# Kernel optimization log

Measured on AMD Instinct MI355X. Metric: run time of the kernel, lower is better.

## Reference

```python
import jax, jax.numpy as jnp
import numpy as np

L = 5          # num_layer
D = 300        # emb_dim
N = 100000     # nodes
E = 250000     # edges
G = 4000       # graphs
EPS = 1e-5


def setup_inputs() -> dict:
    key = jax.random.key(0)
    ks = jax.random.split(key, 32)
    f = lambda k, shape, s=0.02: (jax.random.normal(k, shape, dtype=jnp.float32) * s)
    inp = {
        "x_atom": jax.random.randint(ks[0], (N,), 0, 120),
        "x_chir": jax.random.randint(ks[1], (N,), 0, 3),
        "src": jax.random.randint(ks[2], (E,), 0, N),
        "dst": jax.random.randint(ks[3], (E,), 0, N),
        "edge_type": jax.random.randint(ks[4], (E,), 0, 6),
        "edge_dir": jax.random.randint(ks[5], (E,), 0, 3),
        "batch": jnp.sort(jax.random.randint(ks[6], (N,), 0, G)),
        # node feature embeddings
        "x_emb1": f(ks[7], (120, D), 0.1),
        "x_emb2": f(ks[8], (3, D), 0.1),
        # per-layer GIN params (stacked over L)
        "edge_e1": f(ks[9], (L, 6, D), 0.1),
        "edge_e2": f(ks[10], (L, 3, D), 0.1),
        "mlp_w1": f(ks[11], (L, D, 2 * D)),
        "mlp_b1": jnp.zeros((L, 2 * D), jnp.float32),
        "mlp_w2": f(ks[12], (L, 2 * D, D)),
        "mlp_b2": jnp.zeros((L, D), jnp.float32),
        # BatchNorm (inference mode: running stats)
        "bn_gamma": jnp.ones((L, D), jnp.float32),
        "bn_beta": jnp.zeros((L, D), jnp.float32),
        "bn_mean": f(ks[13], (L, D), 0.1),
        "bn_var": jax.random.uniform(ks[14], (L, D), jnp.float32, 0.5, 1.5),
        # virtual node (embedding initialized to zero in the original)
        "vn_emb": jnp.zeros((D,), jnp.float32),
        # vn MLPs: Linear -> LayerNorm -> ReLU -> Linear, L-1 of them
        "vn_w1": f(ks[15], (L - 1, D, D)),
        "vn_b1": jnp.zeros((L - 1, D), jnp.float32),
        "vn_ln_g": jnp.ones((L - 1, D), jnp.float32),
        "vn_ln_b": jnp.zeros((L - 1, D), jnp.float32),
        "vn_w2": f(ks[16], (L - 1, D, D)),
        "vn_b2": jnp.zeros((L - 1, D), jnp.float32),
    }
    return inp


def _forward(x_atom, x_chir, src, dst, edge_type, edge_dir, batch,
             x_emb1, x_emb2, edge_e1, edge_e2, mlp_w1, mlp_b1, mlp_w2, mlp_b2,
             bn_gamma, bn_beta, bn_mean, bn_var,
             vn_emb, vn_w1, vn_b1, vn_ln_g, vn_ln_b, vn_w2, vn_b2):
    n = x_atom.shape[0]
    # node counts per graph for mean pooling (guard empty graphs)
    counts = jnp.maximum(
        jax.ops.segment_sum(jnp.ones((n, 1), jnp.float32), batch, num_segments=G), 1.0)

    h = x_emb1[x_atom] + x_emb2[x_chir]                      # [N, D]
    vn_h = jnp.broadcast_to(vn_emb, (G, D))                  # [G, D]
    h = h + vn_h[batch]

    for l in range(L):
        # --- GIN conv: message = h[src] + edge_emb, scatter-add to dst ---
        edge_emb = edge_e1[l][edge_type] + edge_e2[l][edge_dir]   # [E, D]
        msg = h[src] + edge_emb
        aggr = jax.ops.segment_sum(msg, dst, num_segments=n)      # [N, D]
        # self loops: x_j = h[i], self-loop attr = (type 4, dir 0)
        aggr = aggr + h + (edge_e1[l][4] + edge_e2[l][0])
        # MLP: Linear(D,2D) -> ReLU -> Linear(2D,D)
        z = jax.nn.relu(aggr @ mlp_w1[l] + mlp_b1[l]) @ mlp_w2[l] + mlp_b2[l]
        # BatchNorm1d (eval): running stats
        z = (z - bn_mean[l]) * (bn_gamma[l] * jax.lax.rsqrt(bn_var[l] + EPS)) + bn_beta[l]
        if l < L - 1:
            z = jax.nn.relu(z)  # (dropout is identity at inference)
            # --- virtual node update ---
            pooled = jax.ops.segment_sum(z, batch, num_segments=G) / counts
            vn_new = pooled + vn_h                                # [G, D]
            t = vn_new @ vn_w1[l] + vn_b1[l]
            mu = jnp.mean(t, axis=-1, keepdims=True)
            var = jnp.var(t, axis=-1, keepdims=True)
            t = (t - mu) * jax.lax.rsqrt(var + EPS) * vn_ln_g[l] + vn_ln_b[l]
            vn_h = jax.nn.relu(t) @ vn_w2[l] + vn_b2[l]
            z = z + vn_h[batch]
        h = z
    return h


def reference(x_atom, x_chir, src, dst, edge_type, edge_dir, batch,
              x_emb1, x_emb2, edge_e1, edge_e2, mlp_w1, mlp_b1, mlp_w2, mlp_b2,
              bn_gamma, bn_beta, bn_mean, bn_var,
              vn_emb, vn_w1, vn_b1, vn_ln_g, vn_ln_b, vn_w2, vn_b2):
    return _forward(x_atom, x_chir, src, dst, edge_type, edge_dir, batch,
                    x_emb1, x_emb2, edge_e1, edge_e2, mlp_w1, mlp_b1, mlp_w2, mlp_b2,
                    bn_gamma, bn_beta, bn_mean, bn_var,
                    vn_emb, vn_w1, vn_b1, vn_ln_g, vn_ln_b, vn_w2, vn_b2)
```

## Files before the change

kernel.cpp:

```cpp
#include <hip/hip_runtime.h>

#define DD   300
#define DD2  600
#define GG   4000
#define GPAD 4096
#define LL   5
#define BN_EPS 1e-5f

typedef float f32x4  __attribute__((ext_vector_type(4)));
typedef short bf16x8 __attribute__((ext_vector_type(8)));

__device__ __forceinline__ unsigned short f2bf(float f) {
    unsigned int x = __float_as_uint(f);
    unsigned int r = (x + 0x7FFFu + ((x >> 16) & 1u)) >> 16;
    return (unsigned short)r;
}

__global__ __launch_bounds__(256) void k_hist(const int* __restrict__ idx, int* __restrict__ cnt, int n) {
    int i = blockIdx.x * 256 + threadIdx.x;
    if (i < n) atomicAdd(&cnt[idx[i]], 1);
}

__global__ __launch_bounds__(256) void k_scan1(const int* __restrict__ in, int* __restrict__ bsum, int n) {
    int t = threadIdx.x;
    int i = blockIdx.x * 256 + t;
    int v = (i < n) ? in[i] : 0;
    for (int off = 32; off >= 1; off >>= 1) v += __shfl_down(v, off, 64);
    __shared__ int s[4];
    if ((t & 63) == 0) s[t >> 6] = v;
    __syncthreads();
    if (t == 0) bsum[blockIdx.x] = s[0] + s[1] + s[2] + s[3];
}
__global__ __launch_bounds__(1024) void k_scan2(int* __restrict__ bsum, int nb) {
    __shared__ int s[1024];
    int t = threadIdx.x;
    int v = (t < nb) ? bsum[t] : 0;
    s[t] = v;
    __syncthreads();
    for (int off = 1; off < 1024; off <<= 1) {
        int u = (t >= off) ? s[t - off] : 0;
        __syncthreads();
        s[t] += u;
        __syncthreads();
    }
    if (t < nb) bsum[t] = s[t] - v;
}
__global__ __launch_bounds__(256) void k_scan3(const int* __restrict__ in, const int* __restrict__ boff,
                                               int* __restrict__ out, int n, int total) {
    __shared__ int s[256];
    int t = threadIdx.x;
    int i = blockIdx.x * 256 + t;
    int v = (i < n) ? in[i] : 0;
    s[t] = v;
    __syncthreads();
    for (int off = 1; off < 256; off <<= 1) {
        int u = (t >= off) ? s[t - off] : 0;
        __syncthreads();
        s[t] += u;
        __syncthreads();
    }
    if (i < n) out[i] = boff[blockIdx.x] + s[t] - v;
    if (i == 0) out[n] = total;
}

__global__ __launch_bounds__(256) void k_place(const int* __restrict__ src, const int* __restrict__ dst,
                                               const int* __restrict__ ety, const int* __restrict__ edir,
                                               const int* __restrict__ rowptr, int* __restrict__ cursor,
                                               int* __restrict__ einfo, int E) {
    int e = blockIdx.x * 256 + threadIdx.x;
    if (e >= E) return;
    int d = dst[e];
    int pos = rowptr[d] + atomicAdd(&cursor[d], 1);
    einfo[pos] = src[e] | ((ety[e] * 3 + edir[e]) << 20);
}

__global__ __launch_bounds__(256) void k_comb(const float* __restrict__ e1, const float* __restrict__ e2,
                                              float* __restrict__ comb) {
    int c = blockIdx.x, l = blockIdx.y;
    const float* r1 = e1 + ((size_t)l * 6 + (c / 3)) * DD;
    const float* r2 = e2 + ((size_t)l * 3 + (c % 3)) * DD;
    float* out = comb + ((size_t)l * 18 + c) * DD;
    for (int d = threadIdx.x; d < DD; d += 256) out[d] = r1[d] + r2[d];
}

__global__ __launch_bounds__(256) void k_init_h(const int* __restrict__ xa, const int* __restrict__ xc,
                                                const float* __restrict__ emb1, const float* __restrict__ emb2,
                                                const float* __restrict__ vne,
                                                float* __restrict__ h, int N) {
    int n = blockIdx.x;
    if (n >= N) return;
    int a = xa[n], c = xc[n];
    for (int d = threadIdx.x; d < DD; d += 256)
        h[(size_t)n * DD + d] = emb1[(size_t)a * DD + d] + emb2[(size_t)c * DD + d] + vne[d];
}

__global__ __launch_bounds__(256) void k_init_vn(const float* __restrict__ vne, float* __restrict__ vnh) {
    int g = blockIdx.x;
    for (int d = threadIdx.x; d < DD; d += 256) vnh[(size_t)g * DD + d] = vne[d];
}

__global__ __launch_bounds__(256) void k_aggr(const float* __restrict__ h,
                                              const int* __restrict__ rowptr, const int* __restrict__ einfo,
                                              const float* __restrict__ comb,
                                              const int* __restrict__ batch, const float* __restrict__ vnh,
                                              int use_vn,
                                              unsigned short* __restrict__ aggrb, int N, int Npad) {
    const int node = blockIdx.x * 4 + (threadIdx.x >> 6);
    const int lane = threadIdx.x & 63;
    if (node >= Npad) return;
    unsigned short* out = aggrb + (size_t)node * 320;
    if (node >= N) {
#pragma unroll
        for (int j = 0; j < 5; j++) out[lane + 64 * j] = 0;
        return;
    }
    float acc[5];
    const float* sc = comb + 12 * DD;
    const int p0 = rowptr[node], p1 = rowptr[node + 1];
    if (use_vn) {
        {
            const float* hs = h + (size_t)node * DD;
            const float* vs = vnh + (size_t)batch[node] * DD;
#pragma unroll
            for (int j = 0; j < 5; j++) {
                int d = lane + 64 * j;
                acc[j] = (d < DD) ? hs[d] + sc[d] + vs[d] : 0.f;
            }
        }
        for (int p = p0; p < p1; p++) {
            int info = einfo[p];
            int s = info & 0xFFFFF;
            const float* hr = h + (size_t)s * DD;
            const float* cr = comb + (size_t)(info >> 20) * DD;
            const float* vr = vnh + (size_t)batch[s] * DD;
#pragma unroll
            for (int j = 0; j < 5; j++) {
                int d = lane + 64 * j;
                if (d < DD) acc[j] += hr[d] + cr[d] + vr[d];
            }
        }
    } else {
        {
            const float* hs = h + (size_t)node * DD;
#pragma unroll
            for (int j = 0; j < 5; j++) {
                int d = lane + 64 * j;
                acc[j] = (d < DD) ? hs[d] + sc[d] : 0.f;
            }
        }
        for (int p = p0; p < p1; p++) {
            int info = einfo[p];
            const float* hr = h + (size_t)(info & 0xFFFFF) * DD;
            const float* cr = comb + (size_t)(info >> 20) * DD;
#pragma unroll
            for (int j = 0; j < 5; j++) {
                int d = lane + 64 * j;
                if (d < DD) acc[j] += hr[d] + cr[d];
            }
        }
    }
#pragma unroll
    for (int j = 0; j < 5; j++) {
        int d = lane + 64 * j;
        out[d] = (d < DD) ? f2bf(acc[j]) : (unsigned short)0;
    }
}

__global__ __launch_bounds__(256) void k_convw(const float* __restrict__ w, short* __restrict__ wt,
                                               int K, int Nn, int KP, int NP) {
    int n = blockIdx.x;
    int l = blockIdx.y;
    const float* wl = w + (size_t)l * K * Nn;
    short* wtl = wt + (size_t)l * NP * KP;
    for (int k = threadIdx.x; k < KP; k += 256) {
        float v = (k < K && n < Nn) ? wl[(size_t)k * Nn + n] : 0.f;
        wtl[(size_t)n * KP + k] = (short)f2bf(v);
    }
}

__global__ __launch_bounds__(256) void k_padb(const float* __restrict__ b, float* __restrict__ bp) {
    int l = blockIdx.y;
    int n = blockIdx.x * 256 + threadIdx.x;
    if (n < 640) bp[(size_t)l * 640 + n] = (n < DD2) ? b[(size_t)l * DD2 + n] : 0.f;
}


#define LD3(PTR, STRIDE, ROWBASE, KOFF)                                                                     \
    do {                                                                                                    \
        v0 = *(const float4*)((PTR) + (size_t)((ROWBASE) + (t >> 2)) * (STRIDE) + (KOFF) + (t & 3) * 8);    \
        v1 = *(const float4*)((PTR) + (size_t)((ROWBASE) + (t >> 2) + 64) * (STRIDE) + (KOFF) + (t & 3) * 8); \
        if (t < 128)                                                                                        \
            v2 = *(const float4*)((PTR) + (size_t)((ROWBASE) + (t >> 2) + 128) * (STRIDE) + (KOFF) + (t & 3) * 8); \
    } while (0)

#define ST3(BUF)                                                    \
    do {                                                            \
        *(float4*)&sB[BUF][t >> 2][(t & 3) * 8] = v0;               \
        *(float4*)&sB[BUF][(t >> 2) + 64][(t & 3) * 8] = v1;        \
        if (t < 128) *(float4*)&sB[BUF][(t >> 2) + 128][(t & 3) * 8] = v2; \
    } while (0)

__global__ __launch_bounds__(256, 2) void k_mlp(const unsigned short* __restrict__ aggrb,
                                                const short* __restrict__ w1t,
                                                const float* __restrict__ b1p,
                                                const short* __restrict__ w2t,
                                                const float* __restrict__ b2,
                                                const float* __restrict__ bng, const float* __restrict__ bnb,
                                                const float* __restrict__ bnm, const float* __restrict__ bnv,
                                                float* __restrict__ h, int N, int relu_out) {
    __shared__ short sH[64][168];
    __shared__ short sB[2][160][40];

    const int t    = threadIdx.x;
    const int m0   = blockIdx.x * 64;
    const int lane = t & 63;
    const int w    = t >> 6;
    const int col  = lane & 15;
    const int kq   = lane >> 4;
    const int kb   = kq << 3;
    const int mrow = (w << 4) + col;

    bf16x8 areg[10];
    {
        const unsigned short* ap = aggrb + (size_t)(m0 + mrow) * 320 + kb;
#pragma unroll
        for (int ks = 0; ks < 10; ks++)
            areg[ks] = *(const bf16x8*)(ap + ks * 32);
        float4 v0, v1, v2;
        LD3(w1t, 320, 0, 0);
        ST3(0);
    }
    __syncthreads();

    f32x4 zacc[20];
#pragma unroll
    for (int j = 0; j < 20; j++) zacc[j] = (f32x4){0.f, 0.f, 0.f, 0.f};

    for (int ch = 0; ch < 4; ch++) {
        f32x4 hacc[10];
#pragma unroll
        for (int j = 0; j < 10; j++) hacc[j] = (f32x4){0.f, 0.f, 0.f, 0.f};

#pragma unroll
        for (int ks = 0; ks < 10; ks++) {
            float4 v0, v1, v2;
            if (ks < 9) LD3(w1t, 320, ch * 160, (ks + 1) * 32);
            else        LD3(w2t, 640, 0, ch * 160);
#pragma unroll
            for (int nt = 0; nt < 10; nt++) {
                bf16x8 b = *(const bf16x8*)&sB[ks & 1][(nt << 4) + col][kb];
                hacc[nt] = __builtin_amdgcn_mfma_f32_16x16x32_bf16(areg[ks], b, hacc[nt], 0, 0, 0);
            }
            ST3((ks & 1) ^ 1);
            if (ks == 9) {
#pragma unroll
                for (int nt = 0; nt < 10; nt++) {
                    float bias = b1p[ch * 160 + (nt << 4) + col];
#pragma unroll
                    for (int r = 0; r < 4; r++)
                        sH[(w << 4) + (kq << 2) + r][(nt << 4) + col] =
                            (short)f2bf(fmaxf(hacc[nt][r] + bias, 0.f));
                }
            }
            __syncthreads();
        }

#pragma unroll
        for (int s = 0; s < 10; s++) {
            const int ks2 = s >> 1, half = s & 1;
            float4 v0, v1, v2;
            bool stage = true;
            if (s < 9)       LD3(w2t, 640, ((s + 1) & 1) * 160, ch * 160 + ((s + 1) >> 1) * 32);
            else if (ch < 3) LD3(w1t, 320, (ch + 1) * 160, 0);
            else stage = false;
            bf16x8 a = *(const bf16x8*)&sH[mrow][ks2 * 32 + kb];
#pragma unroll
            for (int jt = 0; jt < 10; jt++) {
                bf16x8 b = *(const bf16x8*)&sB[s & 1][(jt << 4) + col][kb];
                zacc[half * 10 + jt] = __builtin_amdgcn_mfma_f32_16x16x32_bf16(a, b, zacc[half * 10 + jt], 0, 0, 0);
            }
            if (stage) ST3((s & 1) ^ 1);
            __syncthreads();
        }
    }

#pragma unroll
    for (int j = 0; j < 20; j++) {
        int n = (j << 4) + col;
        if (n < DD) {
            float bz = b2[n];
            float sc = bng[n] * rsqrtf(bnv[n] + BN_EPS);
            float mB = bnm[n], bB = bnb[n];
            int mbase = m0 + (w << 4) + (kq << 2);
#pragma unroll
            for (int r = 0; r < 4; r++) {
                int m = mbase + r;
                if (m < N) {
                    float z = (zacc[j][r] + bz - mB) * sc + bB;
                    if (relu_out) z = fmaxf(z, 0.f);
                    h[(size_t)m * DD + n] = z;
                }
            }
        }
    }
}

__global__ __launch_bounds__(256) void k_pool2(const float* __restrict__ h, const int* __restrict__ gptr,
                                               const float* __restrict__ vnh,
                                               unsigned short* __restrict__ vnin) {
    int g = blockIdx.x, t = threadIdx.x;
    const int gs = gptr[g], ge = gptr[g + 1];
    const float inv = 1.0f / fmaxf((float)(ge - gs), 1.0f);
    const int j0 = t, j1 = t + 256;
    const bool g1 = (j1 < DD);
    float a0 = 0.f, a1 = 0.f;
    for (int n = gs; n < ge; n++) {
        a0 += h[(size_t)n * DD + j0];
        if (g1) a1 += h[(size_t)n * DD + j1];
    }
    vnin[(size_t)g * 320 + j0] = f2bf(a0 * inv + vnh[(size_t)g * DD + j0]);
    if (j1 < 320)
        vnin[(size_t)g * 320 + j1] = g1 ? f2bf(a1 * inv + vnh[(size_t)g * DD + j1]) : (unsigned short)0;
}

__global__ __launch_bounds__(256) void k_vng(const unsigned short* __restrict__ A,
                                             const short* __restrict__ Wt,
                                             const float* __restrict__ bias,
                                             float* __restrict__ outf,
                                             int M) {
    __shared__ short sA[2][64][40];
    __shared__ short sB[2][160][40];
    const int t  = threadIdx.x;
    const int m0 = blockIdx.x * 64;
    const int n0 = blockIdx.y * 160;
    const int ar = t >> 2, aq = (t & 3) << 3;

    {
        *(float4*)&sA[0][ar][aq] = *(const float4*)(A + (size_t)(m0 + ar) * 320 + aq);
#pragma unroll
        for (int i = 0; i < 3; i++) {
            int c = t + (i << 8);
            if (c < 640) {
                int br = c >> 2, bq = (c & 3) << 3;
                *(float4*)&sB[0][br][bq] = *(const float4*)(Wt + (size_t)(n0 + br) * 320 + bq);
            }
        }
    }
    __syncthreads();

    const int lane = t & 63;
    const int w    = t >> 6;
    const int mrow = (w << 4) + (lane & 15);
    const int kb   = (lane >> 4) << 3;
    const int col  = lane & 15;
    const int rq   = (lane >> 4) << 2;

    f32x4 acc[10];
#pragma unroll
    for (int nt = 0; nt < 10; nt++) acc[nt] = (f32x4){0.f, 0.f, 0.f, 0.f};

    for (int ks = 0; ks < 10; ks++) {
        const int nb = ks & 1;
        const bool have = (ks + 1) < 10;
        float4 avr, bv0, bv1, bv2;
        if (have) {
            const int k0 = (ks + 1) << 5;
            avr = *(const float4*)(A + (size_t)(m0 + ar) * 320 + k0 + aq);
            int c = t;
            bv0 = *(const float4*)(Wt + (size_t)(n0 + (c >> 2)) * 320 + k0 + ((c & 3) << 3));
            c = t + 256;
            bv1 = *(const float4*)(Wt + (size_t)(n0 + (c >> 2)) * 320 + k0 + ((c & 3) << 3));
            if (t < 128) {
                c = t + 512;
                bv2 = *(const float4*)(Wt + (size_t)(n0 + (c >> 2)) * 320 + k0 + ((c & 3) << 3));
            }
        }
        bf16x8 a = *(const bf16x8*)&sA[nb][mrow][kb];
#pragma unroll
        for (int nt = 0; nt < 10; nt++) {
            bf16x8 b = *(const bf16x8*)&sB[nb][(nt << 4) + col][kb];
            acc[nt] = __builtin_amdgcn_mfma_f32_16x16x32_bf16(a, b, acc[nt], 0, 0, 0);
        }
        if (have) {
            *(float4*)&sA[nb ^ 1][ar][aq] = avr;
            int c = t;
            *(float4*)&sB[nb ^ 1][c >> 2][(c & 3) << 3] = bv0;
            c = t + 256;
            *(float4*)&sB[nb ^ 1][c >> 2][(c & 3) << 3] = bv1;
            if (t < 128) {
                c = t + 512;
                *(float4*)&sB[nb ^ 1][c >> 2][(c & 3) << 3] = bv2;
            }
        }
        __syncthreads();
    }

#pragma unroll
    for (int nt = 0; nt < 10; nt++) {
        int n = n0 + (nt << 4) + col;
        bool nok = (n < DD);
        float bz = nok ? bias[n] : 0.f;
        int mbase = m0 + (w << 4) + rq;
#pragma unroll
        for (int r = 0; r < 4; r++) {
            int m = mbase + r;
            if (nok && m < M)
                outf[(size_t)m * DD + n] = acc[nt][r] + bz;
        }
    }
}

__global__ __launch_bounds__(256) void k_ln(const float* __restrict__ tbuf,
                                            const float* __restrict__ lng, const float* __restrict__ lnb,
                                            unsigned short* __restrict__ vnrelu) {
    __shared__ float rs[4], rq[4];
    __shared__ float s_mu, s_rstd;
    int g = blockIdx.x, t = threadIdx.x;
    const int j0 = t, j1 = t + 256;
    const bool g1 = (j1 < DD);
    float t0 = tbuf[(size_t)g * DD + j0];
    float t1 = g1 ? tbuf[(size_t)g * DD + j1] : 0.f;
    float ps = t0 + t1;
    float pq = t0 * t0 + t1 * t1;
    for (int off = 32; off >= 1; off >>= 1) { ps += __shfl_down(ps, off, 64); pq += __shfl_down(pq, off, 64); }
    int wid = t >> 6, lane = t & 63;
    if (lane == 0) { rs[wid] = ps; rq[wid] = pq; }
    __syncthreads();
    if (t == 0) {
        float S = rs[0] + rs[1] + rs[2] + rs[3];
        float Q = rq[0] + rq[1] + rq[2] + rq[3];
        float mu = S / DD;
        float var = Q / DD - mu * mu;
        s_mu = mu;
        s_rstd = rsqrtf(var + BN_EPS);
    }
    __syncthreads();
    float mu = s_mu, rstd = s_rstd;
    float r0 = fmaxf((t0 - mu) * rstd * lng[j0] + lnb[j0], 0.f);
    vnrelu[(size_t)g * 320 + j0] = f2bf(r0);
    if (j1 < 320) {
        float r1 = g1 ? fmaxf((t1 - mu) * rstd * lng[j1] + lnb[j1], 0.f) : 0.f;
        vnrelu[(size_t)g * 320 + j1] = g1 ? f2bf(r1) : (unsigned short)0;
    }
}

extern "C" void kernel_launch(void* const* d_in, const int* in_sizes, int n_in,
                              void* d_out, int out_size, void* d_ws, size_t ws_size,
                              hipStream_t stream) {
    const int*   x_atom = (const int*)d_in[0];
    const int*   x_chir = (const int*)d_in[1];
    const int*   src    = (const int*)d_in[2];
    const int*   dst    = (const int*)d_in[3];
    const int*   ety    = (const int*)d_in[4];
    const int*   edir   = (const int*)d_in[5];
    const int*   batch  = (const int*)d_in[6];
    const float* emb1   = (const float*)d_in[7];
    const float* emb2   = (const float*)d_in[8];
    const float* e1     = (const float*)d_in[9];
    const float* e2     = (const float*)d_in[10];
    const float* w1     = (const float*)d_in[11];
    const float* b1     = (const float*)d_in[12];
    const float* w2     = (const float*)d_in[13];
    const float* b2     = (const float*)d_in[14];
    const float* bng    = (const float*)d_in[15];
    const float* bnb    = (const float*)d_in[16];
    const float* bnm    = (const float*)d_in[17];
    const float* bnv    = (const float*)d_in[18];
    const float* vne    = (const float*)d_in[19];
    const float* vw1    = (const float*)d_in[20];
    const float* vb1    = (const float*)d_in[21];
    const float* lng    = (const float*)d_in[22];
    const float* lnb    = (const float*)d_in[23];
    const float* vw2    = (const float*)d_in[24];
    const float* vb2    = (const float*)d_in[25];

    const int N = in_sizes[0];
    const int E = in_sizes[2];
    const int gx = (N + 63) / 64;
    const int Npad = gx * 64;
    const int nbN = (N + 255) / 256;
    const int nbG = (GG + 255) / 256;

    float* h = (float*)d_out;

    unsigned short* aggrb  = (unsigned short*)d_ws;
    unsigned short* hidden = aggrb + (size_t)Npad * 320;
    short*          w1t    = (short*)(hidden + (size_t)Npad * 640);
    short*          w2t    = w1t + (size_t)LL * 640 * 320;
    short*          vw1t   = w2t + (size_t)LL * 320 * 640;
    short*          vw2t   = vw1t + (size_t)(LL - 1) * 320 * 320;
    unsigned short* vnin   = (unsigned short*)(vw2t + (size_t)(LL - 1) * 320 * 320);
    unsigned short* vnrelu = vnin + (size_t)GPAD * 320;
    float*          b1p    = (float*)(vnrelu + (size_t)GPAD * 320);
    float*          comb   = b1p + (size_t)LL * 640;
    float*          tbuf   = comb + (size_t)LL * 18 * DD;
    float*          vnh    = tbuf + (size_t)GG * DD;
    int*            deg    = (int*)(vnh + (size_t)GG * DD);
    int*            cursor = deg + N;
    int*            gcnt   = cursor + N;
    int*            rowptr = gcnt + GG;
    int*            gptr   = rowptr + (N + 1);
    int*            bsumN  = gptr + (GG + 1);
    int*            bsumG  = bsumN + 1024;
    int*            einfo  = bsumG + 1024;

    k_convw<<<dim3(640, LL), 256, 0, stream>>>(w1, w1t, DD, DD2, 320, 640);
    k_convw<<<dim3(320, LL), 256, 0, stream>>>(w2, w2t, DD2, DD, 640, 320);
    k_convw<<<dim3(320, LL - 1), 256, 0, stream>>>(vw1, vw1t, DD, DD, 320, 320);
    k_convw<<<dim3(320, LL - 1), 256, 0, stream>>>(vw2, vw2t, DD, DD, 320, 320);
    k_padb<<<dim3(3, LL), 256, 0, stream>>>(b1, b1p);
    k_comb<<<dim3(18, LL), 256, 0, stream>>>(e1, e2, comb);

    hipMemsetAsync(deg, 0, (size_t)(2 * N + GG) * sizeof(int), stream);
    k_hist<<<(E + 255) / 256, 256, 0, stream>>>(dst, deg, E);
    k_hist<<<(N + 255) / 256, 256, 0, stream>>>(batch, gcnt, N);
    k_scan1<<<nbN, 256, 0, stream>>>(deg, bsumN, N);
    k_scan2<<<1, 1024, 0, stream>>>(bsumN, nbN);
    k_scan3<<<nbN, 256, 0, stream>>>(deg, bsumN, rowptr, N, E);
    k_scan1<<<nbG, 256, 0, stream>>>(gcnt, bsumG, GG);
    k_scan2<<<1, 1024, 0, stream>>>(bsumG, nbG);
    k_scan3<<<nbG, 256, 0, stream>>>(gcnt, bsumG, gptr, GG, N);
    k_place<<<(E + 255) / 256, 256, 0, stream>>>(src, dst, ety, edir, rowptr, cursor, einfo, E);

    k_init_h<<<N, 256, 0, stream>>>(x_atom, x_chir, emb1, emb2, vne, h, N);
    k_init_vn<<<GG, 256, 0, stream>>>(vne, vnh);

    for (int l = 0; l < LL; l++) {
        k_aggr<<<Npad / 4, 256, 0, stream>>>(h, rowptr, einfo, comb + (size_t)l * 18 * DD,
                                             batch, vnh, (l > 0) ? 1 : 0, aggrb, N, Npad);
        k_mlp<<<gx, 256, 0, stream>>>(aggrb, w1t + (size_t)l * 640 * 320,
                                      b1p + (size_t)l * 640,
                                      w2t + (size_t)l * 320 * 640,
                                      b2 + (size_t)l * DD,
                                      bng + (size_t)l * DD, bnb + (size_t)l * DD,
                                      bnm + (size_t)l * DD, bnv + (size_t)l * DD,
                                      h, N, (l < LL - 1) ? 1 : 0);
        if (l < LL - 1) {
            k_pool2<<<GG, 256, 0, stream>>>(h, gptr, vnh, vnin);
            k_vng<<<dim3(GPAD / 64, 2), 256, 0, stream>>>(vnin, vw1t + (size_t)l * 320 * 320,
                                                          vb1 + (size_t)l * DD, tbuf, GG);
            k_ln<<<GG, 256, 0, stream>>>(tbuf, lng + (size_t)l * DD, lnb + (size_t)l * DD, vnrelu);
            k_vng<<<dim3(GPAD / 64, 2), 256, 0, stream>>>(vnrelu, vw2t + (size_t)l * 320 * 320,
                                                          vb2 + (size_t)l * DD, vnh, GG);
        }
    }
}
```

Baseline: 2.126 ms.

## Use 2x2 wave tiling in fused MLP and read weights directly from global

Reorganizes the fused GIN MLP kernel so the four waves form a 2x2 grid over rows and output columns, with each wave computing two 16-row fragments. Weight B-fragments are now loaded straight from global memory (relying on the cache) rather than being double-buffered through shared memory, and the A operand is reloaded from global on each chunk instead of being held in registers. This removes the shared-memory staging and most per-step barriers, and doubles reuse of each B fragment across two row tiles. The cost is more global and L2 traffic for weights, with load latency now exposed directly to the MFMA loop.

```diff
diff --git a/kernel.cpp b/kernel.cpp
--- a/kernel.cpp
+++ b/kernel.cpp
@@ -184,22 +184,6 @@
     if (n < 640) bp[(size_t)l * 640 + n] = (n < DD2) ? b[(size_t)l * DD2 + n] : 0.f;
 }
 
-
-#define LD3(PTR, STRIDE, ROWBASE, KOFF)                                                                     \
-    do {                                                                                                    \
-        v0 = *(const float4*)((PTR) + (size_t)((ROWBASE) + (t >> 2)) * (STRIDE) + (KOFF) + (t & 3) * 8);    \
-        v1 = *(const float4*)((PTR) + (size_t)((ROWBASE) + (t >> 2) + 64) * (STRIDE) + (KOFF) + (t & 3) * 8); \
-        if (t < 128)                                                                                        \
-            v2 = *(const float4*)((PTR) + (size_t)((ROWBASE) + (t >> 2) + 128) * (STRIDE) + (KOFF) + (t & 3) * 8); \
-    } while (0)
-
-#define ST3(BUF)                                                    \
-    do {                                                            \
-        *(float4*)&sB[BUF][t >> 2][(t & 3) * 8] = v0;               \
-        *(float4*)&sB[BUF][(t >> 2) + 64][(t & 3) * 8] = v1;        \
-        if (t < 128) *(float4*)&sB[BUF][(t >> 2) + 128][(t & 3) * 8] = v2; \
-    } while (0)
-
 __global__ __launch_bounds__(256, 2) void k_mlp(const unsigned short* __restrict__ aggrb,
                                                 const short* __restrict__ w1t,
                                                 const float* __restrict__ b1p,
@@ -209,96 +193,102 @@
                                                 const float* __restrict__ bnm, const float* __restrict__ bnv,
                                                 float* __restrict__ h, int N, int relu_out) {
     __shared__ short sH[64][168];
-    __shared__ short sB[2][160][40];
 
     const int t    = threadIdx.x;
     const int m0   = blockIdx.x * 64;
     const int lane = t & 63;
-    const int w    = t >> 6;
+    const int wv   = t >> 6;
+    const int mi   = wv >> 1;
+    const int ni   = wv & 1;
     const int col  = lane & 15;
     const int kq   = lane >> 4;
     const int kb   = kq << 3;
-    const int mrow = (w << 4) + col;
-
-    bf16x8 areg[10];
-    {
-        const unsigned short* ap = aggrb + (size_t)(m0 + mrow) * 320 + kb;
-#pragma unroll
-        for (int ks = 0; ks < 10; ks++)
-            areg[ks] = *(const bf16x8*)(ap + ks * 32);
-        float4 v0, v1, v2;
-        LD3(w1t, 320, 0, 0);
-        ST3(0);
-    }
-    __syncthreads();
-
-    f32x4 zacc[20];
-#pragma unroll
-    for (int j = 0; j < 20; j++) zacc[j] = (f32x4){0.f, 0.f, 0.f, 0.f};
-
+
+    const unsigned short* aA0 = aggrb + (size_t)(m0 + mi * 32 + col) * 320 + kb;
+    const unsigned short* aA1 = aA0 + (size_t)16 * 320;
+    const short* bW2[10];
+#pragma unroll
+    for (int jt = 0; jt < 10; jt++)
+        bW2[jt] = w2t + (size_t)(ni * 160 + jt * 16 + col) * 640 + kb;
+
+    f32x4 zacc[2][10];
+#pragma unroll
+    for (int f = 0; f < 2; f++)
+#pragma unroll
+        for (int j = 0; j < 10; j++) zacc[f][j] = (f32x4){0.f, 0.f, 0.f, 0.f};
+
+#pragma unroll 1
     for (int ch = 0; ch < 4; ch++) {
-        f32x4 hacc[10];
-#pragma unroll
-        for (int j = 0; j < 10; j++) hacc[j] = (f32x4){0.f, 0.f, 0.f, 0.f};
+        f32x4 hacc[2][5];
+#pragma unroll
+        for (int f = 0; f < 2; f++)
+#pragma unroll
+            for (int j = 0; j < 5; j++) hacc[f][j] = (f32x4){0.f, 0.f, 0.f, 0.f};
+
+        const short* bW1[5];
+#pragma unroll
+        for (int nt = 0; nt < 5; nt++)
+            bW1[nt] = w1t + (size_t)(ch * 160 + ni * 80 + nt * 16 + col) * 320 + kb;
 
 #pragma unroll
         for (int ks = 0; ks < 10; ks++) {
-            float4 v0, v1, v2;
-            if (ks < 9) LD3(w1t, 320, ch * 160, (ks + 1) * 32);
-            else        LD3(w2t, 640, 0, ch * 160);
-#pragma unroll
-            for (int nt = 0; nt < 10; nt++) {
-                bf16x8 b = *(const bf16x8*)&sB[ks & 1][(nt << 4) + col][kb];
-                hacc[nt] = __builtin_amdgcn_mfma_f32_16x16x32_bf16(areg[ks], b, hacc[nt], 0, 0, 0);
-            }
-            ST3((ks & 1) ^ 1);
-            if (ks == 9) {
-#pragma unroll
-                for (int nt = 0; nt < 10; nt++) {
-                    float bias = b1p[ch * 160 + (nt << 4) + col];
-#pragma unroll
-                    for (int r = 0; r < 4; r++)
-                        sH[(w << 4) + (kq << 2) + r][(nt << 4) + col] =
-                            (short)f2bf(fmaxf(hacc[nt][r] + bias, 0.f));
-                }
-            }
-            __syncthreads();
-        }
-
-#pragma unroll
-        for (int s = 0; s < 10; s++) {
-            const int ks2 = s >> 1, half = s & 1;
-            float4 v0, v1, v2;
-            bool stage = true;
-            if (s < 9)       LD3(w2t, 640, ((s + 1) & 1) * 160, ch * 160 + ((s + 1) >> 1) * 32);
-            else if (ch < 3) LD3(w1t, 320, (ch + 1) * 160, 0);
-            else stage = false;
-            bf16x8 a = *(const bf16x8*)&sH[mrow][ks2 * 32 + kb];
+            bf16x8 a0 = *(const bf16x8*)(aA0 + ks * 32);
+            bf16x8 a1 = *(const bf16x8*)(aA1 + ks * 32);
+#pragma unroll
+            for (int nt = 0; nt < 5; nt++) {
+                bf16x8 b = *(const bf16x8*)(bW1[nt] + ks * 32);
+                hacc[0][nt] = __builtin_amdgcn_mfma_f32_16x16x32_bf16(a0, b, hacc[0][nt], 0, 0, 0);
+                hacc[1][nt] = __builtin_amdgcn_mfma_f32_16x16x32_bf16(a1, b, hacc[1][nt], 0, 0, 0);
+            }
+        }
+
+        __syncthreads();
+#pragma unroll
+        for (int nt = 0; nt < 5; nt++) {
+            int cc = ni * 80 + nt * 16 + col;
+            float bias = b1p[ch * 160 + cc];
+#pragma unroll
+            for (int f = 0; f < 2; f++) {
+#pragma unroll
+                for (int r = 0; r < 4; r++)
+                    sH[mi * 32 + f * 16 + (kq << 2) + r][cc] =
+                        (short)f2bf(fmaxf(hacc[f][nt][r] + bias, 0.f));
+            }
+        }
+        __syncthreads();
+
+        const int koff = ch * 160;
+#pragma unroll
+        for (int s = 0; s < 5; s++) {
+            bf16x8 ha0 = *(const bf16x8*)&sH[mi * 32 + col][s * 32 + kb];
+            bf16x8 ha1 = *(const bf16x8*)&sH[mi * 32 + 16 + col][s * 32 + kb];
 #pragma unroll
             for (int jt = 0; jt < 10; jt++) {
-                bf16x8 b = *(const bf16x8*)&sB[s & 1][(jt << 4) + col][kb];
-                zacc[half * 10 + jt] = __builtin_amdgcn_mfma_f32_16x16x32_bf16(a, b, zacc[half * 10 + jt], 0, 0, 0);
-            }
-            if (stage) ST3((s & 1) ^ 1);
-            __syncthreads();
-        }
-    }
-
-#pragma unroll
-    for (int j = 0; j < 20; j++) {
-        int n = (j << 4) + col;
+                bf16x8 b = *(const bf16x8*)(bW2[jt] + koff + s * 32);
+                zacc[0][jt] = __builtin_amdgcn_mfma_f32_16x16x32_bf16(ha0, b, zacc[0][jt], 0, 0, 0);
+                zacc[1][jt] = __builtin_amdgcn_mfma_f32_16x16x32_bf16(ha1, b, zacc[1][jt], 0, 0, 0);
+            }
+        }
+    }
+
+#pragma unroll
+    for (int jt = 0; jt < 10; jt++) {
+        int n = ni * 160 + (jt << 4) + col;
         if (n < DD) {
             float bz = b2[n];
             float sc = bng[n] * rsqrtf(bnv[n] + BN_EPS);
             float mB = bnm[n], bB = bnb[n];
-            int mbase = m0 + (w << 4) + (kq << 2);
-#pragma unroll
-            for (int r = 0; r < 4; r++) {
-                int m = mbase + r;
-                if (m < N) {
-                    float z = (zacc[j][r] + bz - mB) * sc + bB;
-                    if (relu_out) z = fmaxf(z, 0.f);
-                    h[(size_t)m * DD + n] = z;
+#pragma unroll
+            for (int f = 0; f < 2; f++) {
+                int mbase = m0 + mi * 32 + f * 16 + (kq << 2);
+#pragma unroll
+                for (int r = 0; r < 4; r++) {
+                    int m = mbase + r;
+                    if (m < N) {
+                        float z = (zacc[f][jt][r] + bz - mB) * sc + bB;
+                        if (relu_out) z = fmaxf(z, 0.f);
+                        h[(size_t)m * DD + n] = z;
+                    }
                 }
             }
         }
```

New measurement: 3.365 ms. +58.3%, slower.

## Retile MLP kernel waves into a 2x2 grid of 32-row by half-column tiles

Applied to the files above, without the earlier changes.

The four waves change from each owning 16 rows across all columns to a 2x2 arrangement: two 32-row halves by two column halves. Each B fragment read from shared memory now feeds two MFMAs, one per 16-row subtile, which halves LDS B-fragment traffic per MFMA. In the second GEMM each wave handles alternate k-steps, selected by a wave-dependent branch. The cost is twice the A registers and a divergent-by-wave branch, and the ch loop is explicitly not unrolled, which could affect register pressure and occupancy.

```diff
diff --git a/kernel.cpp b/kernel.cpp
--- a/kernel.cpp
+++ b/kernel.cpp
@@ -214,32 +214,40 @@
     const int t    = threadIdx.x;
     const int m0   = blockIdx.x * 64;
     const int lane = t & 63;
-    const int w    = t >> 6;
+    const int wv   = t >> 6;
+    const int mi   = wv >> 1;
+    const int ni   = wv & 1;
     const int col  = lane & 15;
     const int kq   = lane >> 4;
     const int kb   = kq << 3;
-    const int mrow = (w << 4) + col;
-
-    bf16x8 areg[10];
+
+    bf16x8 areg[2][10];
     {
-        const unsigned short* ap = aggrb + (size_t)(m0 + mrow) * 320 + kb;
-#pragma unroll
-        for (int ks = 0; ks < 10; ks++)
-            areg[ks] = *(const bf16x8*)(ap + ks * 32);
+        const unsigned short* ap = aggrb + (size_t)(m0 + mi * 32 + col) * 320 + kb;
+#pragma unroll
+        for (int ks = 0; ks < 10; ks++) {
+            areg[0][ks] = *(const bf16x8*)(ap + ks * 32);
+            areg[1][ks] = *(const bf16x8*)(ap + (size_t)16 * 320 + ks * 32);
+        }
         float4 v0, v1, v2;
         LD3(w1t, 320, 0, 0);
         ST3(0);
     }
     __syncthreads();
 
-    f32x4 zacc[20];
-#pragma unroll
-    for (int j = 0; j < 20; j++) zacc[j] = (f32x4){0.f, 0.f, 0.f, 0.f};
-
+    f32x4 zacc[2][10];
+#pragma unroll
+    for (int f = 0; f < 2; f++)
+#pragma unroll
+        for (int j = 0; j < 10; j++) zacc[f][j] = (f32x4){0.f, 0.f, 0.f, 0.f};
+
+#pragma unroll 1
     for (int ch = 0; ch < 4; ch++) {
-        f32x4 hacc[10];
-#pragma unroll
-        for (int j = 0; j < 10; j++) hacc[j] = (f32x4){0.f, 0.f, 0.f, 0.f};
+        f32x4 hacc[2][5];
+#pragma unroll
+        for (int f = 0; f < 2; f++)
+#pragma unroll
+            for (int j = 0; j < 5; j++) hacc[f][j] = (f32x4){0.f, 0.f, 0.f, 0.f};
 
 #pragma unroll
         for (int ks = 0; ks < 10; ks++) {
@@ -247,19 +255,24 @@
             if (ks < 9) LD3(w1t, 320, ch * 160, (ks + 1) * 32);
             else        LD3(w2t, 640, 0, ch * 160);
 #pragma unroll
-            for (int nt = 0; nt < 10; nt++) {
-                bf16x8 b = *(const bf16x8*)&sB[ks & 1][(nt << 4) + col][kb];
-                hacc[nt] = __builtin_amdgcn_mfma_f32_16x16x32_bf16(areg[ks], b, hacc[nt], 0, 0, 0);
+            for (int nt = 0; nt < 5; nt++) {
+                bf16x8 b = *(const bf16x8*)&sB[ks & 1][ni * 80 + (nt << 4) + col][kb];
+                hacc[0][nt] = __builtin_amdgcn_mfma_f32_16x16x32_bf16(areg[0][ks], b, hacc[0][nt], 0, 0, 0);
+                hacc[1][nt] = __builtin_amdgcn_mfma_f32_16x16x32_bf16(areg[1][ks], b, hacc[1][nt], 0, 0, 0);
             }
             ST3((ks & 1) ^ 1);
             if (ks == 9) {
 #pragma unroll
-                for (int nt = 0; nt < 10; nt++) {
-                    float bias = b1p[ch * 160 + (nt << 4) + col];
-#pragma unroll
-                    for (int r = 0; r < 4; r++)
-                        sH[(w << 4) + (kq << 2) + r][(nt << 4) + col] =
-                            (short)f2bf(fmaxf(hacc[nt][r] + bias, 0.f));
+                for (int nt = 0; nt < 5; nt++) {
+                    int cc = ni * 80 + (nt << 4) + col;
+                    float bias = b1p[ch * 160 + cc];
+#pragma unroll
+                    for (int f = 0; f < 2; f++) {
+#pragma unroll
+                        for (int r = 0; r < 4; r++)
+                            sH[mi * 32 + f * 16 + (kq << 2) + r][cc] =
+                                (short)f2bf(fmaxf(hacc[f][nt][r] + bias, 0.f));
+                    }
                 }
             }
             __syncthreads();
@@ -267,17 +280,21 @@
 
 #pragma unroll
         for (int s = 0; s < 10; s++) {
-            const int ks2 = s >> 1, half = s & 1;
+            const int ks2 = s >> 1;
             float4 v0, v1, v2;
             bool stage = true;
             if (s < 9)       LD3(w2t, 640, ((s + 1) & 1) * 160, ch * 160 + ((s + 1) >> 1) * 32);
             else if (ch < 3) LD3(w1t, 320, (ch + 1) * 160, 0);
             else stage = false;
-            bf16x8 a = *(const bf16x8*)&sH[mrow][ks2 * 32 + kb];
-#pragma unroll
-            for (int jt = 0; jt < 10; jt++) {
-                bf16x8 b = *(const bf16x8*)&sB[s & 1][(jt << 4) + col][kb];
-                zacc[half * 10 + jt] = __builtin_amdgcn_mfma_f32_16x16x32_bf16(a, b, zacc[half * 10 + jt], 0, 0, 0);
+            if ((s & 1) == ni) {
+                bf16x8 ha0 = *(const bf16x8*)&sH[mi * 32 + col][ks2 * 32 + kb];
+                bf16x8 ha1 = *(const bf16x8*)&sH[mi * 32 + 16 + col][ks2 * 32 + kb];
+#pragma unroll
+                for (int jt = 0; jt < 10; jt++) {
+                    bf16x8 b = *(const bf16x8*)&sB[s & 1][(jt << 4) + col][kb];
+                    zacc[0][jt] = __builtin_amdgcn_mfma_f32_16x16x32_bf16(ha0, b, zacc[0][jt], 0, 0, 0);
+                    zacc[1][jt] = __builtin_amdgcn_mfma_f32_16x16x32_bf16(ha1, b, zacc[1][jt], 0, 0, 0);
+                }
             }
             if (stage) ST3((s & 1) ^ 1);
             __syncthreads();
@@ -285,20 +302,23 @@
     }
 
 #pragma unroll
-    for (int j = 0; j < 20; j++) {
-        int n = (j << 4) + col;
+    for (int jt = 0; jt < 10; jt++) {
+        int n = ni * 160 + (jt << 4) + col;
         if (n < DD) {
             float bz = b2[n];
             float sc = bng[n] * rsqrtf(bnv[n] + BN_EPS);
             float mB = bnm[n], bB = bnb[n];
-            int mbase = m0 + (w << 4) + (kq << 2);
-#pragma unroll
-            for (int r = 0; r < 4; r++) {
-                int m = mbase + r;
-                if (m < N) {
-                    float z = (zacc[j][r] + bz - mB) * sc + bB;
-                    if (relu_out) z = fmaxf(z, 0.f);
-                    h[(size_t)m * DD + n] = z;
+#pragma unroll
+            for (int f = 0; f < 2; f++) {
+                int mbase = m0 + mi * 32 + f * 16 + (kq << 2);
+#pragma unroll
+                for (int r = 0; r < 4; r++) {
+                    int m = mbase + r;
+                    if (m < N) {
+                        float z = (zacc[f][jt][r] + bz - mB) * sc + bB;
+                        if (relu_out) z = fmaxf(z, 0.f);
+                        h[(size_t)m * DD + n] = z;
+                    }
                 }
             }
         }
```

Result: no change. 2.150 ms (+1.1%).
